# Kernel optimization log

Measured on AMD Instinct MI355X. Metric: run time of the kernel, lower is better.

The kernel has to match this reference:

```python
import jax, jax.numpy as jnp
import numpy as np

DROPOUT_P = 0.5


def normalize_adj(A):
    # A_tilda = A + I ; A_hat = D^-0.5 A_tilda D^-0.5
    # The torch code does this with diag_embed + two bmm (O(N^3));
    # mathematically it is row/col broadcasting (O(N^2)).
    B, N, _ = A.shape
    A_tilda = A + jnp.eye(N, dtype=A.dtype)
    d_inv_sqrt = jnp.sum(A_tilda, axis=2) ** -0.5          # [B, N]
    return d_inv_sqrt[:, :, None] * A_tilda * d_inv_sqrt[:, None, :]


def gcn_layer(X, A_hat, W, b):
    # standard Kipf GCN layer: A_hat @ (X @ W) + b
    return jnp.einsum('bnm,bmd->bnd', A_hat, X @ W) + b


def setup_inputs() -> dict:
    key = jax.random.key(0)
    ks = jax.random.split(key, 6)
    B, N, Din, H, C = 8, 2048, 64, 64, 16
    X = jax.random.normal(ks[0], (B, N, Din), dtype=jnp.float32)
    A = jax.random.uniform(ks[1], (B, N, N), dtype=jnp.float32)
    W1 = jax.random.normal(ks[2], (Din, H), dtype=jnp.float32) * (1.0 / np.sqrt(Din))
    b1 = jax.random.normal(ks[3], (H,), dtype=jnp.float32) * 0.01
    W2 = jax.random.normal(ks[4], (H, C), dtype=jnp.float32) * (1.0 / np.sqrt(H))
    b2 = jax.random.normal(ks[5], (C,), dtype=jnp.float32) * 0.01
    return {"X": X, "A": A, "W1": W1, "b1": b1, "W2": W2, "b2": b2}


def reference(X, A, W1, b1, W2, b2):
    A_hat = normalize_adj(A)
    h = jax.nn.relu(gcn_layer(X, A_hat, W1, b1))
    # F.dropout default training=True -> apply dropout with a fixed key
    keep = jax.random.bernoulli(jax.random.key(42), 1.0 - DROPOUT_P, h.shape)
    h = jnp.where(keep, h / (1.0 - DROPOUT_P), 0.0).astype(h.dtype)
    return gcn_layer(h, A_hat, W2, b2)
```

## Files before the change

kernel.cpp:

```cpp
#include <hip/hip_runtime.h>

#define BN 16384
#define NN 2048
#define DD 64
#define CC 16

typedef short bf16x8 __attribute__((ext_vector_type(8)));
typedef float f32x4 __attribute__((ext_vector_type(4)));
typedef unsigned short u16x4 __attribute__((ext_vector_type(4)));

__device__ __forceinline__ f32x4 mfma16(bf16x8 a, bf16x8 b, f32x4 c) {
  return __builtin_amdgcn_mfma_f32_16x16x32_bf16(a, b, c, 0, 0, 0);
}
__device__ __forceinline__ unsigned short f2bf(float f) {
  unsigned u = __float_as_uint(f);
  return (unsigned short)((u + 0x7FFFu + ((u >> 16) & 1u)) >> 16);
}
__device__ __forceinline__ float bf2f(unsigned short h) {
  return __uint_as_float(((unsigned)h) << 16);
}

__device__ __forceinline__ unsigned tf_bits(unsigned i) {
  unsigned x0 = 0u;
  unsigned x1 = i;
  const unsigned k0 = 0u, k1 = 42u, k2 = 0x1BD11BDAu ^ 0u ^ 42u;
  x0 += k0; x1 += k1;
#define TFR(r) { x0 += x1; x1 = (x1 << (r)) | (x1 >> (32 - (r))); x1 ^= x0; }
  TFR(13) TFR(15) TFR(26) TFR(6)
  x0 += k1; x1 += k2 + 1u;
  TFR(17) TFR(29) TFR(16) TFR(24)
  x0 += k2; x1 += k0 + 2u;
  TFR(13) TFR(15) TFR(26) TFR(6)
  x0 += k0; x1 += k1 + 3u;
  TFR(17) TFR(29) TFR(16) TFR(24)
  x0 += k1; x1 += k2 + 4u;
  TFR(13) TFR(15) TFR(26) TFR(6)
  x0 += k2; x1 += k0 + 5u;
#undef TFR
  return x0 ^ x1;
}


__global__ __launch_bounds__(256) void k_deg(const float* __restrict__ A,
    const float* __restrict__ X, const float* __restrict__ W1,
    float* __restrict__ dis, unsigned short* __restrict__ Abf,
    unsigned short* __restrict__ Y1s, unsigned short* __restrict__ Y1sT)
{
  const int w = threadIdx.x >> 6, lane = threadIdx.x & 63;
  const size_t row = (size_t)blockIdx.x * 4 + w;
  const float4* Arow = (const float4*)(A + row * NN);
  unsigned short* Brow = Abf + row * NN;
  float s = 0.f;
#pragma unroll
  for (int it = 0; it < 8; ++it) {
    float4 v = Arow[lane + 64 * it];
    s += (v.x + v.y) + (v.z + v.w);
    u16x4 p = { f2bf(v.x), f2bf(v.y), f2bf(v.z), f2bf(v.w) };
    *(u16x4*)(Brow + lane * 4 + it * 256) = p;
  }
#pragma unroll
  for (int m = 32; m; m >>= 1) s += __shfl_xor(s, m, 64);
  const float dv = 1.0f / sqrtf(s + 1.0f);
  if (lane == 0) dis[row] = dv;
  const float* Xr = X + row * DD;
  float acc = 0.f;
#pragma unroll
  for (int k = 0; k < DD; ++k) acc += Xr[k] * W1[k * DD + lane];
  const unsigned short yv = f2bf(dv * acc);
  Y1s[row * DD + lane] = yv;
  const int b = (int)(row >> 11), kr = (int)(row & (NN - 1));
  Y1sT[((size_t)b * DD + lane) * NN + kr] = yv;
}

__global__ __launch_bounds__(256, 4) void k_gemm1f(const unsigned short* __restrict__ Abf,
    const unsigned short* __restrict__ Y1sT, const unsigned short* __restrict__ Y1s,
    const float* __restrict__ dis, const float* __restrict__ b1,
    const float* __restrict__ W2,
    unsigned short* __restrict__ Y2sT, float* __restrict__ S2d)
{
  __shared__ float red[4][16][68];
  __shared__ float W2l[DD * CC];
  const int tid = threadIdx.x;
  *(float4*)(W2l + tid * 4) = *(const float4*)(W2 + tid * 4);
  const int Mb = blockIdx.x;
  const int w = __builtin_amdgcn_readfirstlane((int)tid >> 6);
  const int lane = tid & 63;
  const int m15 = lane & 15, quad = lane >> 4;
  const int b = Mb >> 7;
  const int k0 = w * 512 + quad * 8;
  const unsigned short* Ap  = Abf + ((size_t)Mb * 16 + m15) * NN + k0;
  const unsigned short* Bp0 = Y1sT + ((size_t)b * DD + m15) * NN + k0;
  const unsigned short* Bp1 = Bp0 + (size_t)16 * NN;
  const unsigned short* Bp2 = Bp0 + (size_t)32 * NN;
  const unsigned short* Bp3 = Bp0 + (size_t)48 * NN;
  const f32x4 zero = 0.f;
  f32x4 acc[4];
  acc[0] = zero; acc[1] = zero; acc[2] = zero; acc[3] = zero;
  bf16x8 a  = *(const bf16x8*)Ap;
  bf16x8 b0 = *(const bf16x8*)Bp0, b1v = *(const bf16x8*)Bp1;
  bf16x8 b2v = *(const bf16x8*)Bp2, b3v = *(const bf16x8*)Bp3;
#pragma unroll 1
  for (int kk = 0; kk < 16; ++kk) {
    const int off = (kk < 15) ? (kk + 1) * 32 : 0;
    bf16x8 na  = *(const bf16x8*)(Ap + off);
    bf16x8 nb0 = *(const bf16x8*)(Bp0 + off);
    bf16x8 nb1 = *(const bf16x8*)(Bp1 + off);
    bf16x8 nb2 = *(const bf16x8*)(Bp2 + off);
    bf16x8 nb3 = *(const bf16x8*)(Bp3 + off);
    acc[0] = mfma16(a, b0,  acc[0]);
    acc[1] = mfma16(a, b1v, acc[1]);
    acc[2] = mfma16(a, b2v, acc[2]);
    acc[3] = mfma16(a, b3v, acc[3]);
    a = na; b0 = nb0; b1v = nb1; b2v = nb2; b3v = nb3;
  }
#pragma unroll
  for (int ni = 0; ni < 4; ++ni)
#pragma unroll
    for (int r = 0; r < 4; ++r)
      red[w][quad * 4 + r][ni * 16 + m15] = acc[ni][r];
  __syncthreads();
  const int rowl = tid >> 4, c0 = (tid & 15) * 4;
  f32x4 sum = *(const f32x4*)&red[0][rowl][c0];
  sum += *(const f32x4*)&red[1][rowl][c0];
  sum += *(const f32x4*)&red[2][rowl][c0];
  sum += *(const f32x4*)&red[3][rowl][c0];
  const int grow = Mb * 16 + rowl;
  const u16x4 y1d = *(const u16x4*)(Y1s + (size_t)grow * DD + c0);
  const float4 b1q = *(const float4*)(b1 + c0);
  const float dv = dis[grow];
  const unsigned o0 = (unsigned)grow * DD + c0;
  f32x4 hq;
#pragma unroll
  for (int j = 0; j < 4; ++j) {
    const float z = sum[j] + bf2f(y1d[j]);
    const float bj = j == 0 ? b1q.x : j == 1 ? b1q.y : j == 2 ? b1q.z : b1q.w;
    float h = fmaxf(dv * z + bj, 0.f);
    const unsigned bits = tf_bits(o0 + j);
    hq[j] = (bits >> 31) ? 0.f : (h + h);
  }
  __syncthreads();
  *(f32x4*)&red[0][rowl][c0] = hq;
  __syncthreads();
  const float* hrow = &red[0][rowl][0];
  const int c2 = tid & 15;
  float s = 0.f;
#pragma unroll
  for (int k = 0; k < DD; ++k) s += hrow[k] * W2l[k * CC + c2];
  const float y2 = dv * s;
  S2d[(size_t)grow * CC + c2] = y2;
  const int kr = grow & (NN - 1);
  Y2sT[((size_t)b * CC + c2) * NN + kr] = f2bf(y2);
}

__global__ __launch_bounds__(256, 4) void k_gemm2o(const unsigned short* __restrict__ Abf,
    const unsigned short* __restrict__ Y2sT, const float* __restrict__ S2d,
    const float* __restrict__ dis, const float* __restrict__ b2,
    float* __restrict__ out)
{
  __shared__ float red[4][16][20];
  const int Mb = blockIdx.x;
  const int w = __builtin_amdgcn_readfirstlane((int)threadIdx.x >> 6);
  const int lane = threadIdx.x & 63;
  const int m15 = lane & 15, quad = lane >> 4;
  const int b = Mb >> 7;
  const int k0 = w * 512 + quad * 8;
  const unsigned short* Ap = Abf + ((size_t)Mb * 16 + m15) * NN + k0;
  const unsigned short* Bp = Y2sT + ((size_t)b * CC + m15) * NN + k0;
  const f32x4 zero = 0.f;
  f32x4 acc = zero;
  bf16x8 a = *(const bf16x8*)Ap;
  bf16x8 bb = *(const bf16x8*)Bp;
#pragma unroll 1
  for (int kk = 0; kk < 16; ++kk) {
    const int off = (kk < 15) ? (kk + 1) * 32 : 0;
    bf16x8 na = *(const bf16x8*)(Ap + off);
    bf16x8 nbb = *(const bf16x8*)(Bp + off);
    acc = mfma16(a, bb, acc);
    a = na; bb = nbb;
  }
#pragma unroll
  for (int r = 0; r < 4; ++r)
    red[w][quad * 4 + r][m15] = acc[r];
  __syncthreads();
  const int tid = threadIdx.x;
  const int rowl = tid >> 4, c = tid & 15;
  const float sum = red[0][rowl][c] + red[1][rowl][c]
                  + red[2][rowl][c] + red[3][rowl][c];
  const int grow = Mb * 16 + rowl;
  out[(size_t)grow * CC + c] =
      dis[grow] * (sum + S2d[(size_t)grow * CC + c]) + b2[c];
}

#define FKS1 4
#define FKS2 16

__global__ __launch_bounds__(256) void d_deg_xw(const float* __restrict__ A,
    const float* __restrict__ X, const float* __restrict__ W1,
    float* __restrict__ dis, float* __restrict__ Y1s)
{
  const int w = threadIdx.x >> 6, lane = threadIdx.x & 63;
  const int row = __builtin_amdgcn_readfirstlane(blockIdx.x * 4 + w);
  const float4* Arow = (const float4*)(A + (size_t)row * NN);
  float s = 0.f;
#pragma unroll
  for (int it = 0; it < 8; ++it) {
    float4 v = Arow[lane + 64 * it];
    s += v.x + v.y + v.z + v.w;
  }
#pragma unroll
  for (int m = 32; m; m >>= 1) s += __shfl_xor(s, m, 64);
  const float dv = 1.0f / sqrtf(s + 1.0f);
  if (lane == 0) dis[row] = dv;
  const float* Xr = X + (size_t)row * DD;
  float acc = 0.f;
#pragma unroll
  for (int k = 0; k < DD; ++k) acc += Xr[k] * W1[k * DD + lane];
  Y1s[(size_t)row * DD + lane] = dv * acc;
}

__global__ __launch_bounds__(256) void d_gemm1(const float* __restrict__ A,
    const float* __restrict__ Y1s, float* __restrict__ Z1)
{
  const int rb = blockIdx.x >> 2, ks = blockIdx.x & (FKS1 - 1);
  const int lane = threadIdx.x & 63;
  const int c0 = __builtin_amdgcn_readfirstlane((threadIdx.x >> 6) << 4);
  const int row = rb * 64 + lane;
  const int batch = rb >> 5;
  const int KSEG = NN / FKS1;
  const float* Arow = A + (size_t)row * NN + ks * KSEG;
  const float* Yb = Y1s + (size_t)batch * NN * DD + c0;
  const int kbase = ks * KSEG;
  float acc[16];
#pragma unroll
  for (int c = 0; c < 16; ++c) acc[c] = 0.f;
  float4 a0 = *(const float4*)(Arow);
  float4 a1 = *(const float4*)(Arow + 4);
  float4 a2 = *(const float4*)(Arow + 8);
  float4 a3 = *(const float4*)(Arow + 12);
  for (int k = 0; k < KSEG; k += 16) {
    const int kn = (k + 16 < KSEG) ? (k + 16) : 0;
    float4 n0 = *(const float4*)(Arow + kn);
    float4 n1 = *(const float4*)(Arow + kn + 4);
    float4 n2 = *(const float4*)(Arow + kn + 8);
    float4 n3 = *(const float4*)(Arow + kn + 12);
    const float* y0 = Yb + (size_t)(kbase + k) * DD;
    const float av[16] = {a0.x, a0.y, a0.z, a0.w, a1.x, a1.y, a1.z, a1.w,
                          a2.x, a2.y, a2.z, a2.w, a3.x, a3.y, a3.z, a3.w};
#pragma unroll
    for (int j = 0; j < 16; ++j) {
      const float* yr = y0 + j * DD;
#pragma unroll
      for (int c = 0; c < 16; ++c) acc[c] += av[j] * yr[c];
    }
    a0 = n0; a1 = n1; a2 = n2; a3 = n3;
  }
  float* Zp = Z1 + ((size_t)ks * BN + row) * DD + c0;
#pragma unroll
  for (int c = 0; c < 16; c += 4) {
    float4 v; v.x = acc[c]; v.y = acc[c+1]; v.z = acc[c+2]; v.w = acc[c+3];
    *(float4*)(Zp + c) = v;
  }
}

__global__ __launch_bounds__(256) void d_epi1(const float* __restrict__ Z1,
    const float* __restrict__ Y1s, const float* __restrict__ dis,
    const float* __restrict__ b1, const float* __restrict__ W2,
    float* __restrict__ Y2s)
{
  __shared__ float W2l[DD * CC];
  __shared__ float hl[4][DD];
  const int tid = threadIdx.x;
  *(float4*)(W2l + tid * 4) = *(const float4*)(W2 + tid * 4);
  const int w = tid >> 6, lane = tid & 63;
  const int row = blockIdx.x * 4 + w;
  const size_t o = (size_t)row * DD + lane;
  float z = Y1s[o];
#pragma unroll
  for (int p = 0; p < FKS1; ++p) z += Z1[(size_t)p * BN * DD + o];
  const float dv = dis[row];
  float h = fmaxf(dv * z + b1[lane], 0.f);
  const unsigned bits = tf_bits((unsigned)o);
  h = (bits >> 31) ? 0.f : (h + h);
  hl[w][lane] = h;
  __syncthreads();
  const int wr = tid >> 6, l = tid & 63;
  const int c = l & 15, kq = l >> 4;
  float p = 0.f;
#pragma unroll
  for (int kk = 0; kk < 16; ++kk)
    p += hl[wr][kq * 16 + kk] * W2l[(kq * 16 + kk) * CC + c];
  p += __shfl_xor(p, 16, 64);
  p += __shfl_xor(p, 32, 64);
  if (l < 16) {
    const int rg = blockIdx.x * 4 + wr;
    Y2s[(size_t)rg * CC + c] = dis[rg] * p;
  }
}

__global__ __launch_bounds__(256) void d_gemm2(const float* __restrict__ A,
    const float* __restrict__ Y2s, float* __restrict__ Z2)
{
  const int rb = blockIdx.x >> 4, ks = blockIdx.x & (FKS2 - 1);
  const int row = rb * 256 + threadIdx.x;
  const int batch = rb >> 3;
  const int KSEG = NN / FKS2;
  const float* Arow = A + (size_t)row * NN + ks * KSEG;
  const float* Yb = Y2s + (size_t)batch * NN * CC;
  const int kbase = ks * KSEG;
  float acc[16];
#pragma unroll
  for (int c = 0; c < 16; ++c) acc[c] = 0.f;
  float4 a0 = *(const float4*)(Arow);
  float4 a1 = *(const float4*)(Arow + 4);
  for (int k = 0; k < KSEG; k += 8) {
    const int kn = (k + 8 < KSEG) ? (k + 8) : 0;
    float4 n0 = *(const float4*)(Arow + kn);
    float4 n1 = *(const float4*)(Arow + kn + 4);
    const float av[8] = {a0.x, a0.y, a0.z, a0.w, a1.x, a1.y, a1.z, a1.w};
#pragma unroll
    for (int j = 0; j < 8; ++j) {
      const float* yr = Yb + (size_t)(kbase + k + j) * CC;
#pragma unroll
      for (int c = 0; c < 16; ++c) acc[c] += av[j] * yr[c];
    }
    a0 = n0; a1 = n1;
  }
  float* Zp = Z2 + ((size_t)ks * BN + row) * CC;
#pragma unroll
  for (int c = 0; c < 16; c += 4) {
    float4 v; v.x = acc[c]; v.y = acc[c+1]; v.z = acc[c+2]; v.w = acc[c+3];
    *(float4*)(Zp + c) = v;
  }
}

__global__ __launch_bounds__(256) void d_final(const float* __restrict__ Z2,
    const float* __restrict__ Y2s, const float* __restrict__ dis,
    const float* __restrict__ b2, float* __restrict__ out)
{
  const int gid = blockIdx.x * 256 + threadIdx.x;
  const int r = gid >> 2, q = gid & 3;
  const size_t o = (size_t)r * CC + q * 4;
  float4 s = *(const float4*)(Y2s + o);
#pragma unroll
  for (int p = 0; p < FKS2; ++p) {
    const float4 zp = *(const float4*)(Z2 + (size_t)p * BN * CC + o);
    s.x += zp.x; s.y += zp.y; s.z += zp.z; s.w += zp.w;
  }
  const float dv = dis[r];
  const float4 bb = *(const float4*)(b2 + q * 4);
  float4 res;
  res.x = dv * s.x + bb.x;
  res.y = dv * s.y + bb.y;
  res.z = dv * s.z + bb.z;
  res.w = dv * s.w + bb.w;
  *(float4*)(out + o) = res;
}

extern "C" void kernel_launch(void* const* d_in, const int* in_sizes, int n_in,
                              void* d_out, int out_size, void* d_ws, size_t ws_size,
                              hipStream_t stream) {
  const float* X  = (const float*)d_in[0];
  const float* A  = (const float*)d_in[1];
  const float* W1 = (const float*)d_in[2];
  const float* b1 = (const float*)d_in[3];
  const float* W2 = (const float*)d_in[4];
  const float* b2 = (const float*)d_in[5];
  float* out = (float*)d_out;
  char* wsb = (char*)d_ws;

  const size_t NEED = 72941568;
  if (ws_size >= NEED) {
    unsigned short* Abf  = (unsigned short*)wsb;
    unsigned short* Y1s  = (unsigned short*)(wsb + 67108864);
    unsigned short* Y1sT = (unsigned short*)(wsb + 69206016);
    unsigned short* Y2sT = (unsigned short*)(wsb + 71303168);
    float*          S2d  = (float*)(wsb + 71827456);
    float*          dis  = (float*)(wsb + 72876032);

    k_deg   <<<BN / 4,  256, 0, stream>>>(A, X, W1, dis, Abf, Y1s, Y1sT);
    k_gemm1f<<<BN / 16, 256, 0, stream>>>(Abf, Y1sT, Y1s, dis, b1, W2, Y2sT, S2d);
    k_gemm2o<<<1024,    256, 0, stream>>>(Abf, Y2sT, S2d, dis, b2, out);
  } else {
    float* ws  = (float*)d_ws;
    float* dis = ws;
    float* Y1s = ws + 16384;
    float* Z1  = Y1s + (size_t)BN * DD;
    float* Z2  = Z1;
    float* Y2s = Z1 + (size_t)FKS1 * BN * DD;

    d_deg_xw<<<BN / 4,     256, 0, stream>>>(A, X, W1, dis, Y1s);
    d_gemm1 <<<256 * FKS1, 256, 0, stream>>>(A, Y1s, Z1);
    d_epi1  <<<BN / 4,     256, 0, stream>>>(Z1, Y1s, dis, b1, W2, Y2s);
    d_gemm2 <<<64 * FKS2,  256, 0, stream>>>(A, Y2s, Z2);
    d_final <<<256,        256, 0, stream>>>(Z2, Y2s, dis, b2, out);
  }
}
```

Baseline: 270.5 us.

## Fuse three stages into one cooperative kernel with grid-wide syncs

Merges the degree/convert kernel, the first GEMM with its epilogue, and the second GEMM into a single persistent cooperative kernel of 1024 blocks, separated by grid.sync barriers. This removes two kernel launch gaps and the tail drain between stages. In exchange, each block handles 16 rows in the first phase instead of 4. It also depends on all 1024 blocks being co-resident (4 per CU), which is checked through an occupancy query, and falls back to the old three-launch path when that check fails.

```diff
diff --git a/kernel.cpp b/kernel.cpp
--- a/kernel.cpp
+++ b/kernel.cpp
@@ -1,4 +1,7 @@
 #include <hip/hip_runtime.h>
+#include <hip/hip_cooperative_groups.h>
+
+namespace cg = cooperative_groups;
 
 #define BN 16384
 #define NN 2048
@@ -38,6 +41,158 @@
   x0 += k2; x1 += k0 + 5u;
 #undef TFR
   return x0 ^ x1;
+}
+
+__global__ __launch_bounds__(256, 4) void k_fused(
+    const float* __restrict__ A, const float* __restrict__ X,
+    const float* __restrict__ W1, const float* __restrict__ b1,
+    const float* __restrict__ W2, const float* __restrict__ b2,
+    float* __restrict__ dis, unsigned short* __restrict__ Abf,
+    unsigned short* __restrict__ Y1s, unsigned short* __restrict__ Y1sT,
+    unsigned short* __restrict__ Y2sT, float* __restrict__ S2d,
+    float* __restrict__ out)
+{
+  __shared__ float red[4][16][68];
+  __shared__ float W2l[DD * CC];
+  const int tid = threadIdx.x;
+  cg::grid_group grid = cg::this_grid();
+  *(float4*)(W2l + tid * 4) = *(const float4*)(W2 + tid * 4);
+
+  {
+    const int w = tid >> 6, lane = tid & 63;
+#pragma unroll 1
+    for (int rep = 0; rep < 4; ++rep) {
+      const size_t row = (size_t)blockIdx.x * 16 + rep * 4 + w;
+      const float4* Arow = (const float4*)(A + row * NN);
+      unsigned short* Brow = Abf + row * NN;
+      float s = 0.f;
+#pragma unroll
+      for (int it = 0; it < 8; ++it) {
+        float4 v = Arow[lane + 64 * it];
+        s += (v.x + v.y) + (v.z + v.w);
+        u16x4 p = { f2bf(v.x), f2bf(v.y), f2bf(v.z), f2bf(v.w) };
+        *(u16x4*)(Brow + lane * 4 + it * 256) = p;
+      }
+#pragma unroll
+      for (int m = 32; m; m >>= 1) s += __shfl_xor(s, m, 64);
+      const float dv = 1.0f / sqrtf(s + 1.0f);
+      if (lane == 0) dis[row] = dv;
+      const float* Xr = X + row * DD;
+      float acc = 0.f;
+#pragma unroll
+      for (int k = 0; k < DD; ++k) acc += Xr[k] * W1[k * DD + lane];
+      const unsigned short yv = f2bf(dv * acc);
+      Y1s[row * DD + lane] = yv;
+      const int bb = (int)(row >> 11), kr = (int)(row & (NN - 1));
+      Y1sT[((size_t)bb * DD + lane) * NN + kr] = yv;
+    }
+  }
+  grid.sync();
+
+  {
+    const int Mb = blockIdx.x;
+    const int w = __builtin_amdgcn_readfirstlane(tid >> 6);
+    const int lane = tid & 63;
+    const int m15 = lane & 15, quad = lane >> 4;
+    const int b = Mb >> 7;
+    const int k0 = w * 512 + quad * 8;
+    const unsigned short* Ap  = Abf + ((size_t)Mb * 16 + m15) * NN + k0;
+    const unsigned short* Bp0 = Y1sT + ((size_t)b * DD + m15) * NN + k0;
+    const unsigned short* Bp1 = Bp0 + (size_t)16 * NN;
+    const unsigned short* Bp2 = Bp0 + (size_t)32 * NN;
+    const unsigned short* Bp3 = Bp0 + (size_t)48 * NN;
+    const f32x4 zero = 0.f;
+    f32x4 acc[4];
+    acc[0] = zero; acc[1] = zero; acc[2] = zero; acc[3] = zero;
+    bf16x8 a  = *(const bf16x8*)Ap;
+    bf16x8 b0 = *(const bf16x8*)Bp0, b1v = *(const bf16x8*)Bp1;
+    bf16x8 b2v = *(const bf16x8*)Bp2, b3v = *(const bf16x8*)Bp3;
+#pragma unroll 1
+    for (int kk = 0; kk < 16; ++kk) {
+      const int off = (kk < 15) ? (kk + 1) * 32 : 0;
+      bf16x8 na  = *(const bf16x8*)(Ap + off);
+      bf16x8 nb0 = *(const bf16x8*)(Bp0 + off);
+      bf16x8 nb1 = *(const bf16x8*)(Bp1 + off);
+      bf16x8 nb2 = *(const bf16x8*)(Bp2 + off);
+      bf16x8 nb3 = *(const bf16x8*)(Bp3 + off);
+      acc[0] = mfma16(a, b0,  acc[0]);
+      acc[1] = mfma16(a, b1v, acc[1]);
+      acc[2] = mfma16(a, b2v, acc[2]);
+      acc[3] = mfma16(a, b3v, acc[3]);
+      a = na; b0 = nb0; b1v = nb1; b2v = nb2; b3v = nb3;
+    }
+#pragma unroll
+    for (int ni = 0; ni < 4; ++ni)
+#pragma unroll
+      for (int r = 0; r < 4; ++r)
+        red[w][quad * 4 + r][ni * 16 + m15] = acc[ni][r];
+    __syncthreads();
+    const int rowl = tid >> 4, c0 = (tid & 15) * 4;
+    f32x4 sum = *(const f32x4*)&red[0][rowl][c0];
+    sum += *(const f32x4*)&red[1][rowl][c0];
+    sum += *(const f32x4*)&red[2][rowl][c0];
+    sum += *(const f32x4*)&red[3][rowl][c0];
+    const int grow = Mb * 16 + rowl;
+    const u16x4 y1d = *(const u16x4*)(Y1s + (size_t)grow * DD + c0);
+    const float4 b1q = *(const float4*)(b1 + c0);
+    const float dv = dis[grow];
+    const unsigned o0 = (unsigned)grow * DD + c0;
+    f32x4 hq;
+#pragma unroll
+    for (int j = 0; j < 4; ++j) {
+      const float z = sum[j] + bf2f(y1d[j]);
+      const float bj = j == 0 ? b1q.x : j == 1 ? b1q.y : j == 2 ? b1q.z : b1q.w;
+      float h = fmaxf(dv * z + bj, 0.f);
+      const unsigned bits = tf_bits(o0 + j);
+      hq[j] = (bits >> 31) ? 0.f : (h + h);
+    }
+    __syncthreads();
+    *(f32x4*)&red[0][rowl][c0] = hq;
+    __syncthreads();
+    const float* hrow = &red[0][rowl][0];
+    const int c2 = tid & 15;
+    float s = 0.f;
+#pragma unroll
+    for (int k = 0; k < DD; ++k) s += hrow[k] * W2l[k * CC + c2];
+    const float y2 = dv * s;
+    S2d[(size_t)grow * CC + c2] = y2;
+    const int kr = grow & (NN - 1);
+    Y2sT[((size_t)b * CC + c2) * NN + kr] = f2bf(y2);
+  }
+  grid.sync();
+
+  {
+    float (*red2)[16][20] = (float (*)[16][20])&red[0][0][0];
+    const int Mb = blockIdx.x;
+    const int w = __builtin_amdgcn_readfirstlane(tid >> 6);
+    const int lane = tid & 63;
+    const int m15 = lane & 15, quad = lane >> 4;
+    const int b = Mb >> 7;
+    const int k0 = w * 512 + quad * 8;
+    const unsigned short* Ap = Abf + ((size_t)Mb * 16 + m15) * NN + k0;
+    const unsigned short* Bp = Y2sT + ((size_t)b * CC + m15) * NN + k0;
+    f32x4 acc = 0.f;
+    bf16x8 a = *(const bf16x8*)Ap;
+    bf16x8 bb = *(const bf16x8*)Bp;
+#pragma unroll 1
+    for (int kk = 0; kk < 16; ++kk) {
+      const int off = (kk < 15) ? (kk + 1) * 32 : 0;
+      bf16x8 na = *(const bf16x8*)(Ap + off);
+      bf16x8 nbb = *(const bf16x8*)(Bp + off);
+      acc = mfma16(a, bb, acc);
+      a = na; bb = nbb;
+    }
+#pragma unroll
+    for (int r = 0; r < 4; ++r)
+      red2[w][quad * 4 + r][m15] = acc[r];
+    __syncthreads();
+    const int rowl = tid >> 4, c = tid & 15;
+    const float sum = red2[0][rowl][c] + red2[1][rowl][c]
+                    + red2[2][rowl][c] + red2[3][rowl][c];
+    const int grow = Mb * 16 + rowl;
+    out[(size_t)grow * CC + c] =
+        dis[grow] * (sum + S2d[(size_t)grow * CC + c]) + b2[c];
+  }
 }
 
 
@@ -166,8 +321,7 @@
   const int k0 = w * 512 + quad * 8;
   const unsigned short* Ap = Abf + ((size_t)Mb * 16 + m15) * NN + k0;
   const unsigned short* Bp = Y2sT + ((size_t)b * CC + m15) * NN + k0;
-  const f32x4 zero = 0.f;
-  f32x4 acc = zero;
+  f32x4 acc = 0.f;
   bf16x8 a = *(const bf16x8*)Ap;
   bf16x8 bb = *(const bf16x8*)Bp;
 #pragma unroll 1
@@ -377,6 +531,28 @@
     float*          S2d  = (float*)(wsb + 71827456);
     float*          dis  = (float*)(wsb + 72876032);
 
+    static int coop_ok = -1;
+    if (coop_ok < 0) {
+      int nb = 0;
+      hipError_t oe = hipOccupancyMaxActiveBlocksPerMultiprocessor(
+          &nb, k_fused, 256, 0);
+      coop_ok = (oe == hipSuccess && nb >= 4) ? 1 : 0;
+    }
+    if (coop_ok == 1) {
+      const float* Ac = A; const float* Xc = X;
+      const float* W1c = W1; const float* b1c = b1;
+      const float* W2c = W2; const float* b2c = b2;
+      float* disc = dis; unsigned short* Abfc = Abf;
+      unsigned short* Y1sc = Y1s; unsigned short* Y1sTc = Y1sT;
+      unsigned short* Y2sTc = Y2sT; float* S2dc = S2d; float* outc = out;
+      void* args[] = {&Ac, &Xc, &W1c, &b1c, &W2c, &b2c, &disc, &Abfc,
+                      &Y1sc, &Y1sTc, &Y2sTc, &S2dc, &outc};
+      hipError_t e = hipLaunchCooperativeKernel(
+          k_fused, dim3(1024), dim3(256), args, 0u, stream);
+      if (e == hipSuccess) return;
+      coop_ok = 0;
+    }
+
     k_deg   <<<BN / 4,  256, 0, stream>>>(A, X, W1, dis, Abf, Y1s, Y1sT);
     k_gemm1f<<<BN / 16, 256, 0, stream>>>(Abf, Y1sT, Y1s, dis, b1, W2, Y2sT, S2d);
     k_gemm2o<<<1024,    256, 0, stream>>>(Abf, Y2sT, S2d, dis, b2, out);
```

Result: no change. 275.5 us (+1.9%).
